# Performance work log

Hardware: AMD Instinct MI355X
Metric: run time of the kernel (lower is better)

The kernel has to match this reference:

```python
import jax, jax.numpy as jnp
import numpy as np

K = 3          # patch_size
PAD = 1        # (K-1)//2
EPS = 1e-8
STYLE_STRENGTH = 1.0


def _whiten(x):
    # WCT whitening: zero-mean, multiply by Cov^{-1/2} (eigendecomposition)
    B, C, H, W = x.shape
    f = x.reshape(B, C, H * W)
    f = f - f.mean(-1, keepdims=True)
    cov = jnp.einsum('bcn,bdn->bcd', f, f) / (H * W - 1)
    e, v = jnp.linalg.eigh(cov)
    d = 1.0 / jnp.sqrt(jnp.maximum(e, EPS))
    wmat = jnp.einsum('bce,be,bde->bcd', v, d, v)   # V diag(e^-1/2) V^T
    return jnp.einsum('bcd,bdn->bcn', wmat, f).reshape(B, C, H, W)


def _color(x, target):
    # WCT coloring: multiply by style Cov^{1/2}, add style mean
    B, C, H, W = x.shape
    f = x.reshape(B, C, H * W)
    t = target.reshape(B, C, -1)
    tm = t.mean(-1, keepdims=True)
    tc = t - tm
    cov = jnp.einsum('bcn,bdn->bcd', tc, tc) / (tc.shape[-1] - 1)
    e, v = jnp.linalg.eigh(cov)
    d = jnp.sqrt(jnp.maximum(e, 0.0))
    cmat = jnp.einsum('bce,be,bde->bcd', v, d, v)   # V diag(e^1/2) V^T
    out = jnp.einsum('bcd,bdn->bcn', cmat, f) + tm
    return out.reshape(B, C, H, W)


def _extract_patches(x):
    # [B,C,H,W] -> [B,H*W,C,K*K], zero padding, stride 1 (matches torch unfold order)
    B, C, H, W = x.shape
    xp = jnp.pad(x, ((0, 0), (0, 0), (PAD, PAD), (PAD, PAD)))
    pats = jnp.stack([xp[:, :, i:i + H, j:j + W] for i in range(K) for j in range(K)], axis=-1)
    return pats.reshape(B, C, H * W, K * K).transpose(0, 2, 1, 3)


def _style_decorator(content_feature, style_feature):
    nc = _whiten(content_feature)
    ns = _whiten(style_feature)
    B, C, H, W = nc.shape
    P = ns.shape[2] * ns.shape[3]                     # number of style patches
    kern = _extract_patches(ns).reshape(B, P, C * K * K)
    knorm = jnp.linalg.norm(kern, axis=2, keepdims=True) + 1e-5
    cpat = _extract_patches(nc).reshape(B, H * W, C * K * K)
    # conv2d with normalized style kernels == cosine-similarity cross-correlation
    score = jnp.einsum('bqm,bpm->bpq', cpat, kern / knorm)    # [B, P, H*W]
    # binarization_patch_score: per-pixel argmax over style patches (one-hot),
    # then deconv with UNNORMALIZED kernels == gather the winning kernel per pixel
    idx = jnp.argmax(score, axis=1)                           # [B, H*W]
    gathered = jnp.take_along_axis(kern, idx[:, :, None], axis=1)  # [B, H*W, C*K*K]
    G = gathered.reshape(B, H, W, C, K, K).transpose(0, 3, 1, 2, 4, 5)  # [B,C,H,W,K,K]
    # conv_transpose2d(pad=K-1) on zero-padded one-hot == overlap-add of kernels
    full = jnp.zeros((B, C, H + K - 1, W + K - 1), dtype=nc.dtype)
    for dx in range(K):
        for dy in range(K):
            full = full.at[:, :, dx:dx + H, dy:dy + W].add(G[..., dx, dy])
    out = full[:, :, PAD:PAD + H, PAD:PAD + W]
    # norm_deconvolution: overlap counts (static)
    nfull = np.zeros((H + K - 1, W + K - 1), dtype=np.float32)
    for dx in range(K):
        for dy in range(K):
            nfull[dx:dx + H, dy:dy + W] += 1.0
    dn = jnp.asarray(nfull[PAD:PAD + H, PAD:PAD + W])
    reassembled = out / dn
    stylized = _color(reassembled, style_feature)
    return (1.0 - STYLE_STRENGTH) * content_feature + STYLE_STRENGTH * stylized


def setup_inputs() -> dict:
    key = jax.random.key(0)
    k1, k2 = jax.random.split(key)
    return {
        'content_feature': jax.random.normal(k1, (2, 512, 64, 64), dtype=jnp.float32),
        'style_feature': jax.random.normal(k2, (2, 512, 64, 64), dtype=jnp.float32),
    }


def reference(content_feature, style_feature):
    return _style_decorator(content_feature, style_feature)
```

## Files before the change

### kernel.cpp

```cpp
#include <hip/hip_runtime.h>


#define CH    512
#define NPIX  4096
#define HPAD  66
#define PPAD  4356
#define MROWS 4480
#define S0W   4480
#define NS_ITERS 7

typedef unsigned short u16;
typedef _Float16 half8 __attribute__((ext_vector_type(8)));
typedef __attribute__((ext_vector_type(4))) float f32x4;

__device__ __forceinline__ float f16tof(u16 h){
  union { u16 u; _Float16 f; } v; v.u = h; return (float)v.f;
}
__device__ __forceinline__ void split2(float x, u16& h, u16& l){
  _Float16 hf = (_Float16)x;
  float r = (x - (float)hf) * 2048.0f;
  union { u16 u; _Float16 f; } hv, lv;
  hv.f = hf; lv.f = (_Float16)r;
  h = hv.u; l = lv.u;
}
__device__ __forceinline__ void gll16(const void* g, void* l){
  __builtin_amdgcn_global_load_lds((const __attribute__((address_space(1))) unsigned*)g,
                                   (__attribute__((address_space(3))) unsigned*)l,
                                   16, 0, 0);
}
__device__ __forceinline__ f32x4 mfma_f16(half8 a, half8 b, f32x4 c){
  return __builtin_amdgcn_mfma_f32_16x16x32_f16(a, b, c, 0, 0, 0);
}

enum { M_COVP = 0, M_NST = 1, M_X3 = 2, M_WHITEN = 3, M_S0 = 4, M_COLOR = 5 };

struct GP {
  const u16 *Ah, *Al, *Bh, *Bl;
  const u16 *Eh, *El, *Fh, *Fl;
  size_t sAz, sBz;
  float* Cf;
  u16 *Ch, *Cl;
  u16 *Gh, *Gl;
  size_t sCz;
  const float* scales;
  const float* meanv;
  int K;
  int Kit;
};

template<int TILE, int MODE, int KSTEP = 32>
__global__ __launch_bounds__(256, 2)
void gemm_sp(GP p){
  constexpr int MF = TILE / 32;
  constexpr int SLOTS = KSTEP / 8;
  constexpr int TSUB = KSTEP / 32;
  constexpr bool SYM = (MODE == M_NST) || (MODE == M_X3);
  const int z = blockIdx.z;
  int m0, n0;
  int kbase = 0;
  int za = z, zout = z;
  bool mirror = false;
  if constexpr (MODE == M_COVP){
    const int b = blockIdx.x;
    const int xcd = b & 7, w = b >> 3;
    const int zc = xcd*2 + (w & 1);
    const int tile = w >> 1;
    m0 = (tile >> 3)*64; n0 = (tile & 7)*64;
    kbase = (zc & 3) * p.Kit;
    za = zc >> 2; zout = zc;
  } else if constexpr (SYM){
    int bx = blockIdx.x;
    int ty = 0;
    while((ty+1)*(ty+2)/2 <= bx) ++ty;
    int tx = bx - ty*(ty+1)/2;
    m0 = ty*64; n0 = tx*64; mirror = (tx != ty);
  } else if constexpr (MODE == M_S0){
    const int b = blockIdx.x;
    const int v = (b & 7)*154 + (b >> 3);
    if(v >= 1225) return;
    m0 = (v / 35)*128; n0 = (v % 35)*128;
  } else {
    m0 = blockIdx.y*TILE; n0 = blockIdx.x*TILE;
  }

  const u16 *Ah, *Al, *Bh, *Bl;
  if constexpr (MODE == M_X3){
    const size_t zb = (size_t)(z & 3) * CH * CH;
    if(z < 4){ Ah=p.Ah+zb; Al=p.Al+zb; Bh=p.Bh+zb; Bl=p.Bl+zb; }
    else     { Ah=p.Eh+zb; Al=p.El+zb; Bh=p.Fh+zb; Bl=p.Fl+zb; }
  } else {
    Ah = p.Ah + (size_t)za * p.sAz;
    Al = p.Al + (size_t)za * p.sAz;
    Bh = p.Bh + (size_t)za * p.sBz;
    Bl = p.Bl + (size_t)za * p.sBz;
  }

  const int tid = threadIdx.x, ln = tid & 63, wv = tid >> 6;
  const int wm = (wv >> 1) * (TILE/2), wn = (wv & 1) * (TILE/2);
  __shared__ __align__(16) u16 sAh[2][TILE*KSTEP], sAl[2][TILE*KSTEP];
  __shared__ __align__(16) u16 sBh[2][TILE*KSTEP], sBl[2][TILE*KSTEP];
  f32x4 acc1[MF][MF], acc2[MF][MF];
#pragma unroll
  for(int i=0;i<MF;++i)
#pragma unroll
    for(int j=0;j<MF;++j){ acc1[i][j] = (f32x4)0.0f; acc2[i][j] = (f32x4)0.0f; }
  const int K = p.K;

  auto stage = [&](int k0, int buf){
#pragma unroll
    for(int s = tid; s < TILE*SLOTS; s += 256){
      const int row = s / SLOTS, pos = s % SLOTS;
      const int kc = pos ^ ((row >> 2) & (SLOTS-1));
      const size_t ga = (size_t)(m0 + row) * K + k0 + kc*8;
      const size_t gb = (size_t)(n0 + row) * K + k0 + kc*8;
      gll16(Ah + ga, sAh[buf] + s*8);
      gll16(Al + ga, sAl[buf] + s*8);
      gll16(Bh + gb, sBh[buf] + s*8);
      gll16(Bl + gb, sBl[buf] + s*8);
    }
  };

  stage(kbase, 0);
  int cur = 0;
  for(int kk = 0; kk < p.Kit; kk += KSTEP){
    __syncthreads();
    if(kk + KSTEP < p.Kit) stage(kbase + kk + KSTEP, cur ^ 1);
    const u16* pAh = sAh[cur]; const u16* pAl = sAl[cur];
    const u16* pBh = sBh[cur]; const u16* pBl = sBl[cur];
#pragma unroll
    for(int t = 0; t < TSUB; ++t){
      half8 ah[MF], al[MF], bh[MF], bl[MF];
#pragma unroll
      for(int i=0;i<MF;++i){
        const int ra = wm + i*16 + (ln & 15);
        const int rb = wn + i*16 + (ln & 15);
        const int pa = (t*4 + (ln >> 4)) ^ ((ra >> 2) & (SLOTS-1));
        const int pb = (t*4 + (ln >> 4)) ^ ((rb >> 2) & (SLOTS-1));
        const int ofa = ra*KSTEP + pa*8;
        const int ofb = rb*KSTEP + pb*8;
        ah[i] = *(const half8*)(pAh + ofa);
        al[i] = *(const half8*)(pAl + ofa);
        bh[i] = *(const half8*)(pBh + ofb);
        bl[i] = *(const half8*)(pBl + ofb);
      }
#pragma unroll
      for(int i=0;i<MF;++i)
#pragma unroll
        for(int j=0;j<MF;++j){
          acc1[i][j] = mfma_f16(ah[i], bh[j], acc1[i][j]);
          acc2[i][j] = mfma_f16(ah[i], bl[j], acc2[i][j]);
          acc2[i][j] = mfma_f16(al[i], bh[j], acc2[i][j]);
        }
    }
    cur ^= 1;
  }
  u16 *C0 = nullptr, *C1 = nullptr;
  if constexpr (MODE == M_NST){
    const size_t zb = (size_t)z * p.sCz;
    C0 = p.Ch + zb; C1 = p.Cl + zb;
  } else if constexpr (MODE == M_X3){
    const size_t zb = (size_t)(z & 3) * p.sCz;
    if(z < 4){ C0 = p.Ch + zb; C1 = p.Cl + zb; }
    else     { C0 = p.Gh + zb; C1 = p.Gl + zb; }
  }
#pragma unroll
  for(int i=0;i<MF;++i)
#pragma unroll
    for(int j=0;j<MF;++j)
#pragma unroll
      for(int r=0;r<4;++r){
        const int m = m0 + wm + i*16 + (ln >> 4)*4 + r;
        const int n = n0 + wn + j*16 + (ln & 15);
        float v = acc1[i][j][r] + acc2[i][j][r] * (1.0f/2048.0f);
        if constexpr (MODE == M_COVP){
          p.Cf[(size_t)zout * p.sCz + (size_t)m * CH + n] = v;
        } else if constexpr (MODE == M_NST || MODE == M_X3){
          if constexpr (MODE == M_NST) v = -0.5f*v + ((m == n) ? 1.5f : 0.0f);
          u16 h, l; split2(v, h, l);
          C0[(size_t)m*CH + n] = h; C1[(size_t)m*CH + n] = l;
          if(mirror){
            C0[(size_t)n*CH + m] = h; C1[(size_t)n*CH + m] = l;
          }
        } else if constexpr (MODE == M_WHITEN){
          v *= p.scales[z*4 + 3];
          const int prow = ((m >> 6) + 1)*HPAD + (m & 63) + 1;
          u16 h, l; split2(v, h, l);
          const size_t o = (size_t)z*p.sCz + (size_t)prow*CH + n;
          p.Ch[o] = h; p.Cl[o] = l;
        } else if constexpr (MODE == M_S0){
          p.Cf[(size_t)m * S0W + n] = v;
        } else {
          const float sc = p.scales[(2+z)*4 + 2];
          const float mu = p.meanv[(2+z)*CH + m];
          p.Cf[(size_t)z*p.sCz + (size_t)m*NPIX + n] = v*sc + mu;
        }
      }
}

__global__ __launch_bounds__(256)
void cov_reduce_kernel(const float* __restrict__ covp, float* __restrict__ cov,
                       float* __restrict__ rowsum){
  size_t t = (size_t)blockIdx.x * 256 + threadIdx.x;
  int z = (int)(t >> 18);
  size_t e = t & 262143;
  float s = 0.f;
#pragma unroll
  for(int c = 0; c < 4; ++c) s += covp[((size_t)(z*4 + c) << 18) + e];
  s *= (1.0f / 4095.0f);
  cov[t] = s;
  __shared__ float red[256];
  red[threadIdx.x] = fabsf(s); __syncthreads();
  for(int w = 128; w > 0; w >>= 1){
    if(threadIdx.x < w) red[threadIdx.x] += red[threadIdx.x + w];
    __syncthreads();
  }
  if(threadIdx.x == 0){
    int row = (int)(e >> 9);
    atomicAdd(&rowsum[z*512 + row], red[0]);
  }
}

__global__ __launch_bounds__(256)
void scale_fin_kernel(const float* __restrict__ rowsum, float* __restrict__ scales){
  __shared__ float red[256];
  for(int z = 0; z < 4; ++z){
    float m = fmaxf(rowsum[z*512 + threadIdx.x], rowsum[z*512 + 256 + threadIdx.x]);
    red[threadIdx.x] = m; __syncthreads();
    for(int w = 128; w > 0; w >>= 1){
      if(threadIdx.x < w) red[threadIdx.x] = fmaxf(red[threadIdx.x], red[threadIdx.x + w]);
      __syncthreads();
    }
    if(threadIdx.x == 0){
      float c = red[0];
      scales[z*4+0] = c;
      scales[z*4+1] = 1.0f / c;
      scales[z*4+2] = sqrtf(c);
      scales[z*4+3] = rsqrtf(c);
    }
    __syncthreads();
  }
}

__global__ __launch_bounds__(256)
void mean_kernel(const float* __restrict__ content, const float* __restrict__ style,
                 float* __restrict__ meanv){
  int mm = blockIdx.x;
  int z = mm >> 9, c = mm & 511;
  const float* X = ((z < 2) ? content + (size_t)z * CH * NPIX
                            : style   + (size_t)(z - 2) * CH * NPIX) + (size_t)c * NPIX;
  float s = 0.f;
  for(int i = threadIdx.x; i < NPIX; i += 256) s += X[i];
  __shared__ float red[256];
  red[threadIdx.x] = s; __syncthreads();
  for(int w = 128; w > 0; w >>= 1){
    if(threadIdx.x < w) red[threadIdx.x] += red[threadIdx.x + w];
    __syncthreads();
  }
  if(threadIdx.x == 0) meanv[mm] = red[0] * (1.0f / NPIX);
}

__global__ __launch_bounds__(256)
void center_split_kernel(const float* __restrict__ content, const float* __restrict__ style,
                         const float* __restrict__ meanv,
                         u16* __restrict__ Xch, u16* __restrict__ Xcl,
                         u16* __restrict__ XcTh, u16* __restrict__ XcTl){
  int z = blockIdx.z;
  const float* X = (z < 2) ? content + (size_t)z * CH * NPIX
                           : style   + (size_t)(z - 2) * CH * NPIX;
  int p0 = blockIdx.x * 64, c0 = blockIdx.y * 64;
  __shared__ float T[64][65];
  int col = threadIdx.x & 63, rq = threadIdx.x >> 6;
#pragma unroll
  for(int i = 0; i < 16; ++i){
    int r = i*4 + rq;
    int c = c0 + r;
    float v = X[(size_t)c * NPIX + p0 + col] - meanv[z*CH + c];
    u16 h, l; split2(v, h, l);
    size_t o = (size_t)(z*CH + c) * NPIX + p0 + col;
    Xch[o] = h; Xcl[o] = l;
    T[col][r] = v;
  }
  __syncthreads();
#pragma unroll
  for(int i = 0; i < 16; ++i){
    int r = i*4 + rq;
    float v = T[r][col];
    u16 h, l; split2(v, h, l);
    size_t o = (size_t)(z*NPIX + p0 + r) * CH + c0 + col;
    XcTh[o] = h; XcTl[o] = l;
  }
}

__global__ __launch_bounds__(256)
void ns_init_kernel(const float* __restrict__ cov, const float* __restrict__ scales,
                    u16* Yh, u16* Yl, u16* Zh, u16* Zl){
  size_t t = (size_t)blockIdx.x * 256 + threadIdx.x;
  int z = (int)(t >> 18);
  size_t e = t & 262143;
  int row = (int)(e >> 9), col = (int)(e & 511);
  float v = cov[t] * scales[z*4+1];
  u16 h, l; split2(v, h, l);
  Yh[t] = h; Yl[t] = l;
  Zh[t] = (row == col) ? (u16)0x3C00 : (u16)0;
  Zl[t] = 0;
}

__global__ __launch_bounds__(256)
void cn2_kernel(const u16* __restrict__ Wh, const u16* __restrict__ Wl,
                float* __restrict__ cn2){
  int b = blockIdx.y;
  int row = blockIdx.x * 16 + (threadIdx.x >> 4);
  int t = threadIdx.x & 15;
  float s = 0.f;
  if(row < PPAD){
    size_t base = ((size_t)(2 + b) * MROWS + row) * CH;
    for(int ch = t; ch < 64; ch += 16){
      uint4 hv = *(const uint4*)(Wh + base + ch*8);
      uint4 lv = *(const uint4*)(Wl + base + ch*8);
      const unsigned* hw = (const unsigned*)&hv;
      const unsigned* lw = (const unsigned*)&lv;
#pragma unroll
      for(int w = 0; w < 4; ++w){
        float v0 = f16tof((u16)(hw[w] & 0xFFFF)) + f16tof((u16)(lw[w] & 0xFFFF))*(1.0f/2048.0f);
        float v1 = f16tof((u16)(hw[w] >> 16))    + f16tof((u16)(lw[w] >> 16))*(1.0f/2048.0f);
        s = fmaf(v0, v0, s); s = fmaf(v1, v1, s);
      }
    }
  }
  for(int off = 8; off; off >>= 1) s += __shfl_down(s, off, 16);
  if(t == 0 && row < PPAD) cn2[b*PPAD + row] = s;
}

__global__ __launch_bounds__(256)
void rnorm_kernel(const float* __restrict__ cn2, float* __restrict__ rnorm){
  int b = blockIdx.y;
  int p = blockIdx.x * 256 + threadIdx.x;
  int py = p >> 6, px = p & 63;
  const float* c2 = cn2 + (size_t)b * PPAD + (size_t)py * HPAD + px;
  float s = 0.f;
#pragma unroll
  for(int i = 0; i < 3; ++i)
#pragma unroll
    for(int j = 0; j < 3; ++j) s += c2[i * HPAD + j];
  rnorm[b * 4096 + p] = 1.0f / (sqrtf(s) + 1e-5f);
}

__global__ __launch_bounds__(256)
void score_partial_kernel(const float* __restrict__ S0T, const float* __restrict__ rnorm,
                          float* __restrict__ pmax, int* __restrict__ pidx, int b){
  const int blk = blockIdx.x;
  const int xcd = blk & 7, w = blk >> 3;
  const int chunk = xcd*8 + (w & 7);
  const int qg = w >> 3;
  const int t = threadIdx.x;
  const int q0 = qg*512 + t, q1 = q0 + 256;
  const int qc0 = (q0 >> 6)*HPAD + (q0 & 63);
  const int qc1 = (q1 >> 6)*HPAD + (q1 & 63);
  const float* rn = rnorm + b * 4096;
  float b0 = -1e30f, b1 = -1e30f; int i0 = 0, i1 = 0;
  for(int p = chunk*64; p < chunk*64 + 64; ++p){
    const size_t base = (size_t)((p >> 6)*HPAD + (p & 63)) * S0W;
    float s0 = 0.f, s1 = 0.f;
#pragma unroll
    for(int i = 0; i < 3; ++i)
#pragma unroll
      for(int j = 0; j < 3; ++j){
        const size_t d = (size_t)(i*HPAD + j) * (S0W + 1);
        s0 += S0T[base + qc0 + d];
        s1 += S0T[base + qc1 + d];
      }
    const float r = rn[p];
    s0 *= r; s1 *= r;
    if(s0 > b0){ b0 = s0; i0 = p; }
    if(s1 > b1){ b1 = s1; i1 = p; }
  }
  pmax[(size_t)chunk*4096 + q0] = b0; pidx[(size_t)chunk*4096 + q0] = i0;
  pmax[(size_t)chunk*4096 + q1] = b1; pidx[(size_t)chunk*4096 + q1] = i1;
}

__global__ __launch_bounds__(256)
void argmax_merge_kernel(const float* __restrict__ pmax, const int* __restrict__ pidx,
                         int* __restrict__ idx, int b){
  int q = blockIdx.x * 256 + threadIdx.x;
  float best = -1e30f; int bp = 0;
  for(int ch = 0; ch < 64; ++ch){
    float v = pmax[(size_t)ch * 4096 + q];
    if(v > best){ best = v; bp = pidx[(size_t)ch * 4096 + q]; }
  }
  idx[b * 4096 + q] = bp;
}

__global__ __launch_bounds__(256)
void gather_kernel(const u16* __restrict__ Wh, const u16* __restrict__ Wl,
                   const int* __restrict__ idx,
                   u16* __restrict__ RTh, u16* __restrict__ RTl){
  int g = blockIdx.x * 256 + threadIdx.x;
  int cg = g & 63;
  int pix = (g >> 6) & 4095;
  int b = g >> 18;
  int y = pix >> 6, x = pix & 63;
  const int* idxb = idx + b * 4096;
  size_t matbase = (size_t)(2 + b) * MROWS * CH;
  float a8[8] = {0,0,0,0,0,0,0,0};
  int cnt = 0;
#pragma unroll
  for(int i = 0; i < 3; ++i){
    int qy = y + 1 - i;
    if((unsigned)qy >= 64u) continue;
#pragma unroll
    for(int j = 0; j < 3; ++j){
      int qx = x + 1 - j;
      if((unsigned)qx >= 64u) continue;
      int p = idxb[qy * 64 + qx];
      int row = ((p >> 6) + i) * HPAD + (p & 63) + j;
      size_t off = matbase + (size_t)row * CH + cg * 8;
      uint4 hv = *(const uint4*)(Wh + off);
      uint4 lv = *(const uint4*)(Wl + off);
      const unsigned* hw = (const unsigned*)&hv;
      const unsigned* lw = (const unsigned*)&lv;
#pragma unroll
      for(int w = 0; w < 4; ++w){
        a8[2*w]   += f16tof((u16)(hw[w] & 0xFFFF)) + f16tof((u16)(lw[w] & 0xFFFF))*(1.0f/2048.0f);
        a8[2*w+1] += f16tof((u16)(hw[w] >> 16))    + f16tof((u16)(lw[w] >> 16))*(1.0f/2048.0f);
      }
      ++cnt;
    }
  }
  float inv = 1.0f / (float)cnt;
  u16 oh[8], ol[8];
#pragma unroll
  for(int k = 0; k < 8; ++k){
    float v = a8[k] * inv;
    split2(v, oh[k], ol[k]);
  }
  size_t ro = ((size_t)(b * 4096 + pix)) * CH + cg * 8;
  *(uint4*)(RTh + ro) = *(const uint4*)oh;
  *(uint4*)(RTl + ro) = *(const uint4*)ol;
}

extern "C" void kernel_launch(void* const* d_in, const int* in_sizes, int n_in,
                              void* d_out, int out_size, void* d_ws, size_t ws_size,
                              hipStream_t stream){
  (void)in_sizes; (void)n_in; (void)out_size; (void)ws_size;
  const float* content = (const float*)d_in[0];
  const float* style   = (const float*)d_in[1];
  float* out = (float*)d_out;

  char* base = (char*)d_ws;
  size_t off = 0;
  auto take = [&](size_t nbytes) -> char* {
    char* p = base + off;
    off = (off + nbytes + 255) & ~(size_t)255;
    return p;
  };
  const size_t MAT = (size_t)CH*CH*2;
  const size_t FEAT = (size_t)CH*NPIX*2;
  const size_t WMAT = (size_t)MROWS*CH*2;
  const size_t S0SZ = (size_t)MROWS*S0W*4;

  float* meanv  = (float*)take((size_t)4*CH*sizeof(float));
  float* scales = (float*)take(256);
  float* rowsum = (float*)take((size_t)4*CH*sizeof(float));
  float* cov    = (float*)take((size_t)4*CH*CH*sizeof(float));
  u16 *Yh=(u16*)take(4*MAT), *Yl=(u16*)take(4*MAT);
  u16 *Zh=(u16*)take(4*MAT), *Zl=(u16*)take(4*MAT);
  u16 *Th=(u16*)take(4*MAT), *Tl=(u16*)take(4*MAT);
  u16 *Ynh=(u16*)take(4*MAT), *Ynl=(u16*)take(4*MAT);
  u16 *Znh=(u16*)take(4*MAT), *Znl=(u16*)take(4*MAT);
  float* covp = (float*)Yh;
  char* P1 = take(2*(size_t)4*WMAT);
  u16 *Xch=(u16*)P1, *Xcl=(u16*)(P1+4*FEAT);
  u16 *Wh=(u16*)P1,  *Wl=(u16*)(P1+4*WMAT);
  char* P0 = take(S0SZ);
  u16 *XcTh=(u16*)P0, *XcTl=(u16*)(P0+4*FEAT);
  float* S0T = (float*)P0;
  u16 *RTh=(u16*)P0, *RTl=(u16*)(P0+2*FEAT);
  float* cn2    = (float*)take((size_t)2*PPAD*sizeof(float));
  float* rnormb = (float*)take((size_t)2*4096*sizeof(float));
  float* pmax   = (float*)take((size_t)64*4096*sizeof(float));
  int*   pidx   = (int*)  take((size_t)64*4096*sizeof(int));
  int*   idxb   = (int*)  take((size_t)2*4096*sizeof(int));

  hipMemsetAsync(rowsum, 0, (size_t)4*CH*sizeof(float), stream);

  mean_kernel<<<2048, 256, 0, stream>>>(content, style, meanv);
  center_split_kernel<<<dim3(64, 8, 4), 256, 0, stream>>>(content, style, meanv,
                                                          Xch, Xcl, XcTh, XcTl);
  {
    GP g{}; g.Ah=Xch; g.Al=Xcl; g.Bh=Xch; g.Bl=Xcl;
    g.sAz = g.sBz = (size_t)CH*NPIX; g.Cf = covp; g.sCz = (size_t)CH*CH;
    g.K = NPIX; g.Kit = 1024;
    gemm_sp<64, M_COVP, 32><<<dim3(1024), 256, 0, stream>>>(g);
  }
  cov_reduce_kernel<<<4096, 256, 0, stream>>>(covp, cov, rowsum);
  scale_fin_kernel<<<1, 256, 0, stream>>>(rowsum, scales);
  ns_init_kernel<<<4096, 256, 0, stream>>>(cov, scales, Yh, Yl, Zh, Zl);

  u16 *Ach[2]={Yh,Yl}, *Bch[2]={Zh,Zl}, *An[2]={Ynh,Ynl}, *Bn[2]={Znh,Znl};
  for(int it = 0; it < NS_ITERS; ++it){
    GP t{}; t.Ah=Bch[0]; t.Al=Bch[1];
    t.Bh=Ach[0]; t.Bl=Ach[1];
    t.sAz = t.sBz = (size_t)CH*CH; t.Ch=Th; t.Cl=Tl; t.sCz=(size_t)CH*CH;
    t.K = CH; t.Kit = CH;
    gemm_sp<64, M_NST, 64><<<dim3(36, 1, 4), 256, 0, stream>>>(t);
    GP u{}; u.Ah=Ach[0]; u.Al=Ach[1];
    u.Bh=Th; u.Bl=Tl;
    u.Eh=Th; u.El=Tl;
    u.Fh=Bch[0]; u.Fl=Bch[1];
    u.Ch=An[0]; u.Cl=An[1];
    u.Gh=Bn[0]; u.Gl=Bn[1];
    u.sCz=(size_t)CH*CH; u.K = CH; u.Kit = CH;
    gemm_sp<64, M_X3, 64><<<dim3(36, 1, 8), 256, 0, stream>>>(u);
    for(int c = 0; c < 2; ++c){ u16* tmp=Ach[c]; Ach[c]=An[c]; An[c]=tmp;
                                tmp=Bch[c]; Bch[c]=Bn[c]; Bn[c]=tmp; }
  }

  hipMemsetAsync(Wh, 0, 4*WMAT, stream);
  hipMemsetAsync(Wl, 0, 4*WMAT, stream);
  {
    GP w{}; w.Ah=XcTh; w.Al=XcTl; w.sAz=(size_t)NPIX*CH;
    w.Bh=Bch[0]; w.Bl=Bch[1]; w.sBz=(size_t)CH*CH;
    w.Ch=Wh; w.Cl=Wl; w.sCz=(size_t)MROWS*CH; w.scales=scales;
    w.K = CH; w.Kit = CH;
    gemm_sp<128, M_WHITEN, 32><<<dim3(4, 32, 4), 256, 0, stream>>>(w);
  }
  cn2_kernel<<<dim3(273, 2), 256, 0, stream>>>(Wh, Wl, cn2);
  rnorm_kernel<<<dim3(16, 2), 256, 0, stream>>>(cn2, rnormb);

  for(int b = 0; b < 2; ++b){
    GP s{};
    s.Ah = Wh + (size_t)(2+b)*MROWS*CH; s.Al = Wl + (size_t)(2+b)*MROWS*CH;
    s.Bh = Wh + (size_t)b*MROWS*CH;     s.Bl = Wl + (size_t)b*MROWS*CH;
    s.sAz = s.sBz = 0; s.Cf = S0T; s.sCz = 0; s.K = CH; s.Kit = CH;
    gemm_sp<128, M_S0, 32><<<dim3(1232), 256, 0, stream>>>(s);
    score_partial_kernel<<<dim3(512), 256, 0, stream>>>(S0T, rnormb, pmax, pidx, b);
    argmax_merge_kernel<<<16, 256, 0, stream>>>(pmax, pidx, idxb, b);
  }

  gather_kernel<<<2048, 256, 0, stream>>>(Wh, Wl, idxb, RTh, RTl);
  {
    GP c{}; c.Ah = Ach[0] + 2*(size_t)CH*CH; c.Al = Ach[1] + 2*(size_t)CH*CH;
    c.sAz = (size_t)CH*CH;
    c.Bh = RTh; c.Bl = RTl; c.sBz = (size_t)NPIX*CH;
    c.Cf = out; c.sCz = (size_t)CH*NPIX; c.scales = scales; c.meanv = meanv;
    c.K = CH; c.Kit = CH;
    gemm_sp<128, M_COLOR, 32><<<dim3(32, 4, 2), 256, 0, stream>>>(c);
  }
}
```

Baseline: 780.8 us.

## Remap S0/whiten GEMM tiles per XCD and fuse argmax merge via atomicMax keys

The S0 score GEMM block-to-tile mapping is changed so each XCD works on rows m congruent to its id, grouped into 7-column bands. This is meant to improve L2 reuse of the A and B panels within each XCD. The whiten GEMM gets a 1D grid with a similar XCD-aware mapping. The separate argmax merge kernel and the pmax/pidx buffers are replaced by 64-bit packed score/index keys reduced with atomicMax, which needs an extra memset. Ties resolve to the lowest index, matching the old order.

```diff
diff --git a/kernel.cpp b/kernel.cpp
--- a/kernel.cpp
+++ b/kernel.cpp
@@ -55,7 +55,7 @@
   constexpr int SLOTS = KSTEP / 8;
   constexpr int TSUB = KSTEP / 32;
   constexpr bool SYM = (MODE == M_NST) || (MODE == M_X3);
-  const int z = blockIdx.z;
+  int z = blockIdx.z;
   int m0, n0;
   int kbase = 0;
   int za = z, zout = z;
@@ -76,9 +76,22 @@
     m0 = ty*64; n0 = tx*64; mirror = (tx != ty);
   } else if constexpr (MODE == M_S0){
     const int b = blockIdx.x;
-    const int v = (b & 7)*154 + (b >> 3);
-    if(v >= 1225) return;
-    m0 = (v / 35)*128; n0 = (v % 35)*128;
+    const int x = b & 7, w = b >> 3;
+    const int R = (x < 3) ? 5 : 4;
+    if(w >= R*35) return;
+    const int g   = w / (R*7);
+    const int rem = w - g*(R*7);
+    const int mi = rem / 7, ni = rem % 7;
+    m0 = (x + mi*8) * 128;
+    n0 = (g*7 + ni) * 128;
+  } else if constexpr (MODE == M_WHITEN){
+    const int b = blockIdx.x;
+    const int x = b & 7, w = b >> 3;
+    z = x >> 1;
+    const int mt = (x & 1) + (w >> 2) * 2;
+    m0 = mt * 128;
+    n0 = (w & 3) * 128;
+    za = z; zout = z;
   } else {
     m0 = blockIdx.y*TILE; n0 = blockIdx.x*TILE;
   }
@@ -345,9 +358,15 @@
   rnorm[b * 4096 + p] = 1.0f / (sqrtf(s) + 1e-5f);
 }
 
+__device__ __forceinline__ unsigned long long score_key(float s, int p){
+  unsigned u = __float_as_uint(s);
+  u = (u & 0x80000000u) ? ~u : (u | 0x80000000u);
+  return ((unsigned long long)u << 32) | (unsigned long long)(0xFFFFFFFFu - (unsigned)p);
+}
+
 __global__ __launch_bounds__(256)
 void score_partial_kernel(const float* __restrict__ S0T, const float* __restrict__ rnorm,
-                          float* __restrict__ pmax, int* __restrict__ pidx, int b){
+                          unsigned long long* __restrict__ skey, int b){
   const int blk = blockIdx.x;
   const int xcd = blk & 7, w = blk >> 3;
   const int chunk = xcd*8 + (w & 7);
@@ -374,32 +393,20 @@
     if(s0 > b0){ b0 = s0; i0 = p; }
     if(s1 > b1){ b1 = s1; i1 = p; }
   }
-  pmax[(size_t)chunk*4096 + q0] = b0; pidx[(size_t)chunk*4096 + q0] = i0;
-  pmax[(size_t)chunk*4096 + q1] = b1; pidx[(size_t)chunk*4096 + q1] = i1;
-}
-
-__global__ __launch_bounds__(256)
-void argmax_merge_kernel(const float* __restrict__ pmax, const int* __restrict__ pidx,
-                         int* __restrict__ idx, int b){
-  int q = blockIdx.x * 256 + threadIdx.x;
-  float best = -1e30f; int bp = 0;
-  for(int ch = 0; ch < 64; ++ch){
-    float v = pmax[(size_t)ch * 4096 + q];
-    if(v > best){ best = v; bp = pidx[(size_t)ch * 4096 + q]; }
-  }
-  idx[b * 4096 + q] = bp;
+  atomicMax(skey + (size_t)b*4096 + q0, score_key(b0, i0));
+  atomicMax(skey + (size_t)b*4096 + q1, score_key(b1, i1));
 }
 
 __global__ __launch_bounds__(256)
 void gather_kernel(const u16* __restrict__ Wh, const u16* __restrict__ Wl,
-                   const int* __restrict__ idx,
+                   const unsigned long long* __restrict__ skey,
                    u16* __restrict__ RTh, u16* __restrict__ RTl){
   int g = blockIdx.x * 256 + threadIdx.x;
   int cg = g & 63;
   int pix = (g >> 6) & 4095;
   int b = g >> 18;
   int y = pix >> 6, x = pix & 63;
-  const int* idxb = idx + b * 4096;
+  const unsigned long long* kb = skey + (size_t)b * 4096;
   size_t matbase = (size_t)(2 + b) * MROWS * CH;
   float a8[8] = {0,0,0,0,0,0,0,0};
   int cnt = 0;
@@ -411,7 +418,7 @@
     for(int j = 0; j < 3; ++j){
       int qx = x + 1 - j;
       if((unsigned)qx >= 64u) continue;
-      int p = idxb[qy * 64 + qx];
+      int p = (int)(0xFFFFFFFFu - (unsigned)(kb[qy * 64 + qx] & 0xFFFFFFFFull));
       int row = ((p >> 6) + i) * HPAD + (p & 63) + j;
       size_t off = matbase + (size_t)row * CH + cg * 8;
       uint4 hv = *(const uint4*)(Wh + off);
@@ -477,11 +484,10 @@
   u16 *RTh=(u16*)P0, *RTl=(u16*)(P0+2*FEAT);
   float* cn2    = (float*)take((size_t)2*PPAD*sizeof(float));
   float* rnormb = (float*)take((size_t)2*4096*sizeof(float));
-  float* pmax   = (float*)take((size_t)64*4096*sizeof(float));
-  int*   pidx   = (int*)  take((size_t)64*4096*sizeof(int));
-  int*   idxb   = (int*)  take((size_t)2*4096*sizeof(int));
+  unsigned long long* skey = (unsigned long long*)take((size_t)2*4096*8);
 
   hipMemsetAsync(rowsum, 0, (size_t)4*CH*sizeof(float), stream);
+  hipMemsetAsync(skey, 0, (size_t)2*4096*8, stream);
 
   mean_kernel<<<2048, 256, 0, stream>>>(content, style, meanv);
   center_split_kernel<<<dim3(64, 8, 4), 256, 0, stream>>>(content, style, meanv,
@@ -522,7 +528,7 @@
     w.Bh=Bch[0]; w.Bl=Bch[1]; w.sBz=(size_t)CH*CH;
     w.Ch=Wh; w.Cl=Wl; w.sCz=(size_t)MROWS*CH; w.scales=scales;
     w.K = CH; w.Kit = CH;
-    gemm_sp<128, M_WHITEN, 32><<<dim3(4, 32, 4), 256, 0, stream>>>(w);
+    gemm_sp<128, M_WHITEN, 32><<<dim3(512), 256, 0, stream>>>(w);
   }
   cn2_kernel<<<dim3(273, 2), 256, 0, stream>>>(Wh, Wl, cn2);
   rnorm_kernel<<<dim3(16, 2), 256, 0, stream>>>(cn2, rnormb);
@@ -532,12 +538,11 @@
     s.Ah = Wh + (size_t)(2+b)*MROWS*CH; s.Al = Wl + (size_t)(2+b)*MROWS*CH;
     s.Bh = Wh + (size_t)b*MROWS*CH;     s.Bl = Wl + (size_t)b*MROWS*CH;
     s.sAz = s.sBz = 0; s.Cf = S0T; s.sCz = 0; s.K = CH; s.Kit = CH;
-    gemm_sp<128, M_S0, 32><<<dim3(1232), 256, 0, stream>>>(s);
-    score_partial_kernel<<<dim3(512), 256, 0, stream>>>(S0T, rnormb, pmax, pidx, b);
-    argmax_merge_kernel<<<16, 256, 0, stream>>>(pmax, pidx, idxb, b);
-  }
-
-  gather_kernel<<<2048, 256, 0, stream>>>(Wh, Wl, idxb, RTh, RTl);
+    gemm_sp<128, M_S0, 32><<<dim3(1400), 256, 0, stream>>>(s);
+    score_partial_kernel<<<dim3(512), 256, 0, stream>>>(S0T, rnormb, skey, b);
+  }
+
+  gather_kernel<<<2048, 256, 0, stream>>>(Wh, Wl, skey, RTh, RTl);
   {
     GP c{}; c.Ah = Ach[0] + 2*(size_t)CH*CH; c.Al = Ach[1] + 2*(size_t)CH*CH;
     c.sAz = (size_t)CH*CH;
```

New measurement: 732.3 us. -6.2%, faster.
